# Kernel tuning notes

Hardware: AMD Instinct MI355X
Metric: run time of the kernel (lower is better)

Reference implementation:

```python
import jax, jax.numpy as jnp
import numpy as np

DIM = 512

def setup_inputs() -> dict:
    key = jax.random.key(0)
    ks = jax.random.split(key, 7)
    B, Nq, Nkv = 8, 1024, 4096
    prototype = jax.random.normal(ks[0], (B, Nq, DIM), dtype=jnp.float32)
    q_x = jax.random.normal(ks[1], (B, Nkv, DIM), dtype=jnp.float32)
    qry_attn_mask = jax.random.bernoulli(ks[2], 0.5, (B, Nkv))  # True = keep
    # Linear(dim, dim, bias=False) weights, torch convention y = x @ W.T
    s = 1.0 / np.sqrt(DIM)
    Wq = jax.random.uniform(ks[3], (DIM, DIM), jnp.float32, -s, s)
    Wk = jax.random.uniform(ks[4], (DIM, DIM), jnp.float32, -s, s)
    Wv = jax.random.uniform(ks[5], (DIM, DIM), jnp.float32, -s, s)
    Wproj = jax.random.uniform(ks[6], (DIM, DIM), jnp.float32, -s, s)
    return {"prototype": prototype, "q_x": q_x, "qry_attn_mask": qry_attn_mask,
            "Wq": Wq, "Wk": Wk, "Wv": Wv, "Wproj": Wproj}

def reference(prototype, q_x, qry_attn_mask, Wq, Wk, Wv, Wproj):
    scale = DIM ** (-0.5)
    q = jnp.einsum('bnd,ed->bne', prototype, Wq)          # [B,Nq,D]
    k = jnp.einsum('bmd,ed->bme', q_x, Wk)                # [B,Nkv,D]
    v = jnp.einsum('bmd,ed->bme', q_x, Wv)                # [B,Nkv,D]
    attn = jnp.einsum('bnd,bmd->bnm', q, k) * scale       # [B,Nq,Nkv]
    bias = (~qry_attn_mask).astype(attn.dtype)[:, None, :] * -10000.0
    attn = jax.nn.softmax(attn + bias, axis=-1)
    x = jnp.einsum('bnm,bmd->bnd', attn, v)
    x = jnp.einsum('bnd,ed->bne', x, Wproj)
    return x
```

## Files before the change

### kernel.cpp

```cpp
#include <hip/hip_runtime.h>
#include <hip/hip_bf16.h>
#include <stdint.h>


typedef __bf16 bf16;
typedef bf16 bf16x8 __attribute__((ext_vector_type(8)));
typedef bf16 bf16x4 __attribute__((ext_vector_type(4)));
typedef float f32x4 __attribute__((ext_vector_type(4)));

#define NB 8
#define NQ 1024
#define NKV 4096
#define DD 512
#define RT_LD 136

__device__ __forceinline__ void direct16(const void* g, void* s) {
  __builtin_amdgcn_global_load_lds(
      (const __attribute__((address_space(1))) void*)g,
      (__attribute__((address_space(3))) void*)s, 16, 0, 0);
}

__global__ void cvt_kernel(const float* __restrict__ src, bf16* __restrict__ dst, int n4) {
  int i = blockIdx.x * blockDim.x + threadIdx.x;
  if (i < n4) {
    float4 v = ((const float4*)src)[i];
    bf16x4 o;
    o.x = (bf16)v.x; o.y = (bf16)v.y; o.z = (bf16)v.z; o.w = (bf16)v.w;
    ((bf16x4*)dst)[i] = o;
  }
}

__global__ void cvt_weights(const float* __restrict__ Wq, const float* __restrict__ Wk,
                            const float* __restrict__ Wv, const float* __restrict__ Wp,
                            bf16* __restrict__ Wq_b, bf16* __restrict__ Wkv_b,
                            bf16* __restrict__ Wp_b) {
  int i = blockIdx.x * blockDim.x + threadIdx.x;
  int w = i >> 16, r = i & 65535;
  const float* src = (w == 0) ? Wq : (w == 1) ? Wk : (w == 2) ? Wv : Wp;
  bf16x4* dst = (w == 0) ? (bf16x4*)Wq_b
              : (w == 3) ? (bf16x4*)Wp_b
                         : (bf16x4*)Wkv_b + (w == 2 ? 65536 : 0);
  float4 v = ((const float4*)src)[r];
  bf16x4 o;
  o.x = (bf16)v.x; o.y = (bf16)v.y; o.z = (bf16)v.z; o.w = (bf16)v.w;
  dst[r] = o;
}

__global__ void sniff_zero(const unsigned* __restrict__ mask, int* __restrict__ flag,
                           float* __restrict__ denom) {
  __shared__ int s_bad0, s_bad1;
  if (threadIdx.x == 0) { s_bad0 = 0; s_bad1 = 0; }
  __syncthreads();
  int b0 = 0, b1 = 0;
  for (int i = threadIdx.x; i < 8192; i += 256) {
    unsigned v = mask[i];
    if (v > 1u) b0 = 1;
    if (v != 0u && v != 0x3F800000u) b1 = 1;
  }
  if (b0) atomicOr(&s_bad0, 1);
  if (b1) atomicOr(&s_bad1, 1);
  for (int i = threadIdx.x; i < NB * NQ; i += 256) denom[i] = 0.f;
  __syncthreads();
  if (threadIdx.x == 0) *flag = (s_bad0 == 0) ? 0 : ((s_bad1 == 0) ? 1 : 2);
}

__global__ void scan_mask(const void* __restrict__ mask, const int* __restrict__ flagP,
                          int* __restrict__ idx, int* __restrict__ cnt,
                          int* __restrict__ kpad) {
  const int b = blockIdx.x, tid = threadIdx.x;
  const int mode = *flagP;
  __shared__ int ps[256];
  unsigned bits = 0;
  int c = 0;
  const int base = tid * 16;
  for (int i = 0; i < 16; ++i) {
    const int col = base + i;
    bool k;
    if (mode == 0)      k = ((const int*)mask)[b * NKV + col] != 0;
    else if (mode == 1) k = ((const float*)mask)[b * NKV + col] != 0.f;
    else                k = ((const unsigned char*)mask)[b * NKV + col] != 0;
    bits |= (unsigned)k << i;
    c += k;
  }
  ps[tid] = c;
  __syncthreads();
  for (int s = 1; s < 256; s <<= 1) {
    int v = (tid >= s) ? ps[tid - s] : 0;
    __syncthreads();
    ps[tid] += v;
    __syncthreads();
  }
  int off = ps[tid] - c;
  for (int i = 0; i < 16; ++i)
    if ((bits >> i) & 1) idx[b * NKV + off++] = base + i;
  if (tid == 255) {
    cnt[b] = ps[255];
    kpad[b] = (ps[255] + 127) & ~127;
  }
}

__global__ void gather_qx(const float* __restrict__ qx, const int* __restrict__ idx,
                          const int* __restrict__ cnt, bf16* __restrict__ qc) {
  const int b = blockIdx.y;
  const int wave = threadIdx.x >> 6, lane = threadIdx.x & 63;
  const int r0 = blockIdx.x * 16 + wave * 4;
  const int n = cnt[b];
#pragma unroll
  for (int j = 0; j < 4; ++j) {
    const int row = r0 + j;
    if (row >= n) return;
    const int src = idx[b * NKV + row];
    const float4* s = (const float4*)(qx + ((long)b * NKV + src) * DD) + lane;
    bf16x4* d = (bf16x4*)(qc + ((long)b * NKV + row) * DD) + lane;
    float4 v0 = s[0], v1 = s[64];
    bf16x4 o0, o1;
    o0.x = (bf16)v0.x; o0.y = (bf16)v0.y; o0.z = (bf16)v0.z; o0.w = (bf16)v0.w;
    o1.x = (bf16)v1.x; o1.y = (bf16)v1.y; o1.z = (bf16)v1.z; o1.w = (bf16)v1.w;
    d[0] = o0;
    d[64] = o1;
  }
}

template <int EPI>
__global__ void __launch_bounds__(256, 2)
gemm_bt(const bf16* __restrict__ A, const bf16* __restrict__ Bw,
        void* __restrict__ Cp, void* __restrict__ Cp2,
        int N, int Klen, int Kstride,
        long sA, long sB, long sC,
        const int* __restrict__ cnt, const int* __restrict__ kpad,
        float* __restrict__ denom, float scale, int M) {
  __shared__ alignas(16) bf16 Smem[128 * RT_LD];
  bf16* As = Smem;
  bf16* Bs = Smem + 4096;
  bf16* Rt = Smem;
  const int tid = threadIdx.x;
  const int wave = tid >> 6, lane = tid & 63;
  const int l15 = lane & 15, l4 = lane >> 4;
  const int wm = (wave >> 1) * 64, wn = (wave & 1) * 64;
  const int bx = (EPI == 5) ? blockIdx.y : blockIdx.x;
  const int by = (EPI == 5) ? blockIdx.x : blockIdx.y;
  const int b = blockIdx.z;

  if constexpr (EPI == 2) {
    if (bx * 128 >= kpad[b]) return;
  } else {
    const int bb = by >> 5, loc = (by & 31) * 128;
    if (loc >= kpad[bb]) return;
  }

  const bf16* Ab = A + (long)b * sA + (long)(by * 128) * Kstride;
  const bf16* Bb = Bw + (long)b * sB + (long)(bx * 128) * Kstride;

  const int c0 = wave * 2, c1 = wave * 2 + 1;
  const int srow = lane >> 2;
  const int scol = (lane & 3) * 8;
  const bf16* ag0 = Ab + (long)(c0 * 16 + srow) * Kstride + scol;
  const bf16* ag1 = Ab + (long)(c1 * 16 + srow) * Kstride + scol;
  const bf16* bg0 = Bb + (long)(c0 * 16 + srow) * Kstride + scol;
  const bf16* bg1 = Bb + (long)(c1 * 16 + srow) * Kstride + scol;
  bf16* al0 = As + c0 * 512 + lane * 8;
  bf16* al1 = As + c1 * 512 + lane * 8;
  bf16* bl0 = Bs + c0 * 512 + lane * 8;
  bf16* bl1 = Bs + c1 * 512 + lane * 8;

  f32x4 acc[4][4] = {};

  for (int kt = 0; kt < Klen; kt += 32) {
    __syncthreads();
    direct16(ag0, al0);
    direct16(ag1, al1);
    direct16(bg0, bl0);
    direct16(bg1, bl1);
    ag0 += 32; ag1 += 32; bg0 += 32; bg1 += 32;
    __syncthreads();
    bf16x8 af[4], bfr[4];
#pragma unroll
    for (int t = 0; t < 4; ++t)
      af[t] = *(const bf16x8*)(As + (wm + t * 16 + l15) * 32 + l4 * 8);
#pragma unroll
    for (int t = 0; t < 4; ++t)
      bfr[t] = *(const bf16x8*)(Bs + (wn + t * 16 + l15) * 32 + l4 * 8);
#pragma unroll
    for (int mt = 0; mt < 4; ++mt)
#pragma unroll
      for (int nt = 0; nt < 4; ++nt)
        acc[mt][nt] = __builtin_amdgcn_mfma_f32_16x16x32_bf16(af[mt], bfr[nt],
                                                              acc[mt][nt], 0, 0, 0);
  }

  const int rowBase = by * 128 + wm;
  const int colBase = bx * 128 + wn;
  const int tR = by * 128;
  const int tC = bx * 128;

  if constexpr (EPI == 2) {
    __syncthreads();
    bf16* C = (bf16*)Cp + (long)b * sC;
    const int nkeep = cnt[b];
    float rs[4][4];
#pragma unroll
    for (int mt = 0; mt < 4; ++mt)
#pragma unroll
      for (int r = 0; r < 4; ++r) rs[mt][r] = 0.f;
#pragma unroll
    for (int nt = 0; nt < 4; ++nt) {
      const bool keep = (colBase + nt * 16 + l15) < nkeep;
#pragma unroll
      for (int mt = 0; mt < 4; ++mt)
#pragma unroll
        for (int r = 0; r < 4; ++r) {
          float p = keep ? __expf(acc[mt][nt][r] * scale) : 0.f;
          rs[mt][r] += p;
          Rt[(wm + mt * 16 + l4 * 4 + r) * RT_LD + wn + nt * 16 + l15] = (bf16)p;
        }
    }
#pragma unroll
    for (int mt = 0; mt < 4; ++mt)
#pragma unroll
      for (int r = 0; r < 4; ++r) {
        float v = rs[mt][r];
        v += __shfl_xor(v, 1, 64);
        v += __shfl_xor(v, 2, 64);
        v += __shfl_xor(v, 4, 64);
        v += __shfl_xor(v, 8, 64);
        if (l15 == 0)
          atomicAdd(&denom[b * M + rowBase + mt * 16 + l4 * 4 + r], v);
      }
    __syncthreads();
    const int r0 = tid >> 2, cq = (tid & 3) * 32;
#pragma unroll
    for (int h = 0; h < 128; h += 64)
#pragma unroll
      for (int j = 0; j < 4; ++j) {
        bf16x8 v = *(const bf16x8*)(Rt + (r0 + h) * RT_LD + cq + j * 8);
        *(bf16x8*)(C + (long)(tR + r0 + h) * N + tC + cq + j * 8) = v;
      }
  } else {
    __syncthreads();
    if (tC < 512) {
      bf16* C = (bf16*)Cp;
#pragma unroll
      for (int mt = 0; mt < 4; ++mt)
#pragma unroll
        for (int nt = 0; nt < 4; ++nt)
#pragma unroll
          for (int r = 0; r < 4; ++r)
            Rt[(wm + mt * 16 + l4 * 4 + r) * RT_LD + wn + nt * 16 + l15] =
                (bf16)acc[mt][nt][r];
      __syncthreads();
      const int r0 = tid >> 2, cq = (tid & 3) * 32;
#pragma unroll
      for (int h = 0; h < 128; h += 64)
#pragma unroll
        for (int j = 0; j < 4; ++j) {
          bf16x8 v = *(const bf16x8*)(Rt + (r0 + h) * RT_LD + cq + j * 8);
          *(bf16x8*)(C + (long)(tR + r0 + h) * 512 + tC + cq + j * 8) = v;
        }
    } else {
      bf16* C = (bf16*)Cp2;
#pragma unroll
      for (int mt = 0; mt < 4; ++mt) {
        const int r0 = wm + mt * 16 + l4 * 4;
#pragma unroll
        for (int nt = 0; nt < 4; ++nt) {
          const int cloc = wn + nt * 16 + l15;
          bf16x4 o;
          o.x = (bf16)acc[mt][nt][0]; o.y = (bf16)acc[mt][nt][1];
          o.z = (bf16)acc[mt][nt][2]; o.w = (bf16)acc[mt][nt][3];
          *(bf16x4*)(Rt + cloc * RT_LD + r0) = o;
        }
      }
      __syncthreads();
      const int bb = tR >> 12, kvloc = tR & 4095;
      const int d0 = tid >> 2, kvq = (tid & 3) * 32;
#pragma unroll
      for (int h = 0; h < 128; h += 64)
#pragma unroll
        for (int j = 0; j < 4; ++j) {
          bf16x8 v = *(const bf16x8*)(Rt + (d0 + h) * RT_LD + kvq + j * 8);
          *(bf16x8*)(C + (long)bb * DD * NKV + (long)(tC - 512 + d0 + h) * NKV +
                     kvloc + kvq + j * 8) = v;
        }
    }
  }
}

template <int EPI>
__global__ void __launch_bounds__(256, 4)
gemm_n64(const bf16* __restrict__ A, const bf16* __restrict__ Bw,
         void* __restrict__ Cp) {
  constexpr int SME = (EPI == 0) ? 128 * 72 : 6144;
  __shared__ alignas(16) bf16 Smem[SME];
  bf16* As = Smem;
  bf16* Bs = Smem + 4096;
  bf16* Rt = Smem;
  const int tid = threadIdx.x;
  const int wave = tid >> 6, lane = tid & 63;
  const int l15 = lane & 15, l4 = lane >> 4;
  const int wm = (wave >> 1) * 64, wn = (wave & 1) * 32;

  const bf16* Ab = A + (long)(blockIdx.y * 128) * DD;
  const bf16* Bb = Bw + (long)(blockIdx.x * 64) * DD;

  const int srow = lane >> 2, scol = (lane & 3) * 8;
  const bf16* ag0 = Ab + (long)(wave * 32 + srow) * DD + scol;
  const bf16* ag1 = ag0 + 16 * DD;
  const bf16* bg0 = Bb + (long)(wave * 16 + srow) * DD + scol;
  bf16* al0 = As + wave * 1024 + lane * 8;
  bf16* al1 = al0 + 512;
  bf16* bl0 = Bs + wave * 512 + lane * 8;

  f32x4 acc[4][2] = {};

  for (int kt = 0; kt < DD; kt += 32) {
    __syncthreads();
    direct16(ag0, al0);
    direct16(ag1, al1);
    direct16(bg0, bl0);
    ag0 += 32; ag1 += 32; bg0 += 32;
    __syncthreads();
    bf16x8 af[4], bfr[2];
#pragma unroll
    for (int t = 0; t < 4; ++t)
      af[t] = *(const bf16x8*)(As + (wm + t * 16 + l15) * 32 + l4 * 8);
#pragma unroll
    for (int t = 0; t < 2; ++t)
      bfr[t] = *(const bf16x8*)(Bs + (wn + t * 16 + l15) * 32 + l4 * 8);
#pragma unroll
    for (int mt = 0; mt < 4; ++mt)
#pragma unroll
      for (int nt = 0; nt < 2; ++nt)
        acc[mt][nt] = __builtin_amdgcn_mfma_f32_16x16x32_bf16(af[mt], bfr[nt],
                                                              acc[mt][nt], 0, 0, 0);
  }

  const int tR = blockIdx.y * 128, tC = blockIdx.x * 64;
  if constexpr (EPI == 0) {
    __syncthreads();
#pragma unroll
    for (int mt = 0; mt < 4; ++mt)
#pragma unroll
      for (int nt = 0; nt < 2; ++nt)
#pragma unroll
        for (int r = 0; r < 4; ++r)
          Rt[(wm + mt * 16 + l4 * 4 + r) * 72 + wn + nt * 16 + l15] =
              (bf16)acc[mt][nt][r];
    __syncthreads();
    bf16* C = (bf16*)Cp;
    const int r0 = tid >> 1, cq = (tid & 1) * 32;
#pragma unroll
    for (int j = 0; j < 4; ++j) {
      bf16x8 v = *(const bf16x8*)(Rt + r0 * 72 + cq + j * 8);
      *(bf16x8*)(C + (long)(tR + r0) * DD + tC + cq + j * 8) = v;
    }
  } else {
    float* C = (float*)Cp;
#pragma unroll
    for (int mt = 0; mt < 4; ++mt)
#pragma unroll
      for (int nt = 0; nt < 2; ++nt)
#pragma unroll
        for (int r = 0; r < 4; ++r)
          C[(long)(tR + wm + mt * 16 + l4 * 4 + r) * DD + tC + wn + nt * 16 + l15] =
              acc[mt][nt][r];
  }
}

__global__ void __launch_bounds__(256, 4)
pv_direct(const bf16* __restrict__ P, const bf16* __restrict__ vT,
          const float* __restrict__ denom, const int* __restrict__ kpad,
          bf16* __restrict__ x) {
  __shared__ alignas(16) bf16 Smem[64 * RT_LD];
  bf16* As = Smem;
  bf16* Bs = Smem + 2048;
  bf16* Rt = Smem;
  const int tid = threadIdx.x;
  const int wave = tid >> 6, lane = tid & 63;
  const int l15 = lane & 15, l4 = lane >> 4;
  const int wm = (wave >> 1) * 32, wn = (wave & 1) * 64;
  const int qB = blockIdx.x * 64;
  const int dB = blockIdx.y * 128;
  const int b = blockIdx.z;
  const int Kb = kpad[b];

  const bf16* Ab = P + (long)b * NQ * NKV + (long)qB * NKV;
  const bf16* Bb = vT + (long)b * DD * NKV + (long)dB * NKV;

  const int srow = lane >> 2, scol = (lane & 3) * 8;
  const bf16* ag = Ab + (long)(wave * 16 + srow) * NKV + scol;
  const bf16* bg0 = Bb + (long)(wave * 32 + srow) * NKV + scol;
  const bf16* bg1 = bg0 + 16 * NKV;
  bf16* al = As + wave * 512 + lane * 8;
  bf16* bl0 = Bs + wave * 1024 + lane * 8;
  bf16* bl1 = bl0 + 512;

  f32x4 acc[2][4] = {};

  for (int kt = 0; kt < Kb; kt += 32) {
    __syncthreads();
    direct16(ag, al);
    direct16(bg0, bl0);
    direct16(bg1, bl1);
    ag += 32; bg0 += 32; bg1 += 32;
    __syncthreads();
    bf16x8 af[2], bfr[4];
#pragma unroll
    for (int t = 0; t < 2; ++t)
      af[t] = *(const bf16x8*)(As + (wm + t * 16 + l15) * 32 + l4 * 8);
#pragma unroll
    for (int t = 0; t < 4; ++t)
      bfr[t] = *(const bf16x8*)(Bs + (wn + t * 16 + l15) * 32 + l4 * 8);
#pragma unroll
    for (int mt = 0; mt < 2; ++mt)
#pragma unroll
      for (int nt = 0; nt < 4; ++nt)
        acc[mt][nt] = __builtin_amdgcn_mfma_f32_16x16x32_bf16(af[mt], bfr[nt],
                                                              acc[mt][nt], 0, 0, 0);
  }

  __syncthreads();
#pragma unroll
  for (int mt = 0; mt < 2; ++mt)
#pragma unroll
    for (int r = 0; r < 4; ++r) {
      const int row = wm + mt * 16 + l4 * 4 + r;
      const float inv = 1.0f / denom[b * NQ + qB + row];
#pragma unroll
      for (int nt = 0; nt < 4; ++nt)
        Rt[row * RT_LD + wn + nt * 16 + l15] = (bf16)(acc[mt][nt][r] * inv);
    }
  __syncthreads();
  const int r0 = tid >> 2, cq = (tid & 3) * 32;
#pragma unroll
  for (int j = 0; j < 4; ++j) {
    bf16x8 v = *(const bf16x8*)(Rt + r0 * RT_LD + cq + j * 8);
    *(bf16x8*)(x + (long)(b * NQ + qB + r0) * DD + dB + cq + j * 8) = v;
  }
}

extern "C" void kernel_launch(void* const* d_in, const int* in_sizes, int n_in,
                              void* d_out, int out_size, void* d_ws, size_t ws_size,
                              hipStream_t stream) {
  const float* proto = (const float*)d_in[0];
  const float* qx    = (const float*)d_in[1];
  const void*  mask  = d_in[2];
  const float* Wq    = (const float*)d_in[3];
  const float* Wk    = (const float*)d_in[4];
  const float* Wv    = (const float*)d_in[5];
  const float* Wproj = (const float*)d_in[6];
  float* out = (float*)d_out;

  char* w = (char*)d_ws;
  int*   flag  = (int*)w;
  int*   cnt   = (int*)(w + 64);
  int*   kpadA = (int*)(w + 128);
  float* denom = (float*)(w + 4096);
  size_t off = 65536;
  bf16* Wq_b  = (bf16*)(w + off); off += (size_t)DD * DD * 2;
  bf16* Wkv_b = (bf16*)(w + off); off += (size_t)DD * DD * 4;
  bf16* Wp_b  = (bf16*)(w + off); off += (size_t)DD * DD * 2;
  int*  idx   = (int*)(w + off);  off += (size_t)NB * NKV * 4;
  bf16* q_b   = (bf16*)(w + off); off += (size_t)NB * NQ * DD * 2;
  bf16* k_b   = (bf16*)(w + off); off += (size_t)NB * NKV * DD * 2;
  bf16* vT_b  = (bf16*)(w + off); off += (size_t)NB * NKV * DD * 2;
  bf16* x_b   = (bf16*)(w + off); off += (size_t)NB * NQ * DD * 2;
  size_t off_pp = off;
  bf16* proto_b = (bf16*)(w + off); off += (size_t)NB * NQ * DD * 2;
  bf16* qc_b    = (bf16*)(w + off);
  bf16* P       = (bf16*)(w + off_pp);

  sniff_zero<<<1, 256, 0, stream>>>((const unsigned*)mask, flag, denom);
  scan_mask<<<8, 256, 0, stream>>>(mask, flag, idx, cnt, kpadA);

  cvt_kernel<<<NB * NQ * DD / 4 / 256, 256, 0, stream>>>(proto, proto_b, NB * NQ * DD / 4);
  gather_qx<<<dim3(NKV / 16, NB), 256, 0, stream>>>(qx, idx, cnt, qc_b);
  cvt_weights<<<4 * 65536 / 256, 256, 0, stream>>>(Wq, Wk, Wv, Wproj, Wq_b, Wkv_b, Wp_b);

  const float scale = 0.04419417382415922f;

  gemm_n64<0><<<dim3(8, 64, 1), 256, 0, stream>>>(proto_b, Wq_b, q_b);
  gemm_bt<5><<<dim3(256, 8, 1), 256, 0, stream>>>(
      qc_b, Wkv_b, k_b, vT_b, 1024, DD, DD, 0L, 0L, 0L,
      cnt, kpadA, nullptr, 0.f, 0);
  gemm_bt<2><<<dim3(NKV / 128, NQ / 128, NB), 256, 0, stream>>>(
      q_b, k_b, P, nullptr, NKV, DD, DD,
      (long)NQ * DD, (long)NKV * DD, (long)NQ * NKV,
      cnt, kpadA, denom, scale, NQ);
  pv_direct<<<dim3(16, 4, 8), 256, 0, stream>>>(P, vT_b, denom, kpadA, x_b);
  gemm_n64<4><<<dim3(8, 64, 1), 256, 0, stream>>>(x_b, Wp_b, out);
}
```

Baseline: 341.6 us.

## Halve gemm_bt epilogue LDS via two-pass staging and shrink PV tile to 32 rows

The gemm_bt epilogue now stages the 128x128 output tile through LDS in two 64-row (or 64-column) halves. This halves the shared-memory footprint and lets launch bounds rise to 4 blocks per CU. The pv_direct kernel drops from 64 to 32 query rows per block, doubling the grid and cutting LDS use to give more parallelism across CUs. The cost is extra barriers in the epilogue, and in PV each V tile load is amortised over fewer rows, which raises global traffic for vT.

```diff
diff --git a/kernel.cpp b/kernel.cpp
--- a/kernel.cpp
+++ b/kernel.cpp
@@ -122,14 +122,14 @@
 }
 
 template <int EPI>
-__global__ void __launch_bounds__(256, 2)
+__global__ void __launch_bounds__(256, 4)
 gemm_bt(const bf16* __restrict__ A, const bf16* __restrict__ Bw,
         void* __restrict__ Cp, void* __restrict__ Cp2,
         int N, int Klen, int Kstride,
         long sA, long sB, long sC,
         const int* __restrict__ cnt, const int* __restrict__ kpad,
         float* __restrict__ denom, float scale, int M) {
-  __shared__ alignas(16) bf16 Smem[128 * RT_LD];
+  __shared__ alignas(16) bf16 Smem[64 * RT_LD];
   bf16* As = Smem;
   bf16* Bs = Smem + 4096;
   bf16* Rt = Smem;
@@ -193,94 +193,106 @@
   const int tR = by * 128;
   const int tC = bx * 128;
 
+  __syncthreads();
+
   if constexpr (EPI == 2) {
-    __syncthreads();
     bf16* C = (bf16*)Cp + (long)b * sC;
     const int nkeep = cnt[b];
-    float rs[4][4];
-#pragma unroll
-    for (int mt = 0; mt < 4; ++mt)
-#pragma unroll
-      for (int r = 0; r < 4; ++r) rs[mt][r] = 0.f;
-#pragma unroll
-    for (int nt = 0; nt < 4; ++nt) {
-      const bool keep = (colBase + nt * 16 + l15) < nkeep;
-#pragma unroll
-      for (int mt = 0; mt < 4; ++mt)
-#pragma unroll
-        for (int r = 0; r < 4; ++r) {
-          float p = keep ? __expf(acc[mt][nt][r] * scale) : 0.f;
-          rs[mt][r] += p;
-          Rt[(wm + mt * 16 + l4 * 4 + r) * RT_LD + wn + nt * 16 + l15] = (bf16)p;
+#pragma unroll
+    for (int h2 = 0; h2 < 2; ++h2) {
+      if (wm == h2 * 64) {
+        float rs[4][4];
+#pragma unroll
+        for (int mt = 0; mt < 4; ++mt)
+#pragma unroll
+          for (int r = 0; r < 4; ++r) rs[mt][r] = 0.f;
+#pragma unroll
+        for (int nt = 0; nt < 4; ++nt) {
+          const bool keep = (colBase + nt * 16 + l15) < nkeep;
+#pragma unroll
+          for (int mt = 0; mt < 4; ++mt)
+#pragma unroll
+            for (int r = 0; r < 4; ++r) {
+              float p = keep ? __expf(acc[mt][nt][r] * scale) : 0.f;
+              rs[mt][r] += p;
+              Rt[(mt * 16 + l4 * 4 + r) * RT_LD + wn + nt * 16 + l15] = (bf16)p;
+            }
         }
+#pragma unroll
+        for (int mt = 0; mt < 4; ++mt)
+#pragma unroll
+          for (int r = 0; r < 4; ++r) {
+            float v = rs[mt][r];
+            v += __shfl_xor(v, 1, 64);
+            v += __shfl_xor(v, 2, 64);
+            v += __shfl_xor(v, 4, 64);
+            v += __shfl_xor(v, 8, 64);
+            if (l15 == 0)
+              atomicAdd(&denom[b * M + rowBase + mt * 16 + l4 * 4 + r], v);
+          }
+      }
+      __syncthreads();
+      const int r0 = tid >> 2, cq = (tid & 3) * 32;
+#pragma unroll
+      for (int j = 0; j < 4; ++j) {
+        bf16x8 v = *(const bf16x8*)(Rt + r0 * RT_LD + cq + j * 8);
+        *(bf16x8*)(C + (long)(tR + h2 * 64 + r0) * N + tC + cq + j * 8) = v;
+      }
+      __syncthreads();
     }
-#pragma unroll
-    for (int mt = 0; mt < 4; ++mt)
-#pragma unroll
-      for (int r = 0; r < 4; ++r) {
-        float v = rs[mt][r];
-        v += __shfl_xor(v, 1, 64);
-        v += __shfl_xor(v, 2, 64);
-        v += __shfl_xor(v, 4, 64);
-        v += __shfl_xor(v, 8, 64);
-        if (l15 == 0)
-          atomicAdd(&denom[b * M + rowBase + mt * 16 + l4 * 4 + r], v);
-      }
-    __syncthreads();
-    const int r0 = tid >> 2, cq = (tid & 3) * 32;
-#pragma unroll
-    for (int h = 0; h < 128; h += 64)
-#pragma unroll
-      for (int j = 0; j < 4; ++j) {
-        bf16x8 v = *(const bf16x8*)(Rt + (r0 + h) * RT_LD + cq + j * 8);
-        *(bf16x8*)(C + (long)(tR + r0 + h) * N + tC + cq + j * 8) = v;
-      }
   } else {
-    __syncthreads();
     if (tC < 512) {
       bf16* C = (bf16*)Cp;
 #pragma unroll
-      for (int mt = 0; mt < 4; ++mt)
-#pragma unroll
-        for (int nt = 0; nt < 4; ++nt)
-#pragma unroll
-          for (int r = 0; r < 4; ++r)
-            Rt[(wm + mt * 16 + l4 * 4 + r) * RT_LD + wn + nt * 16 + l15] =
-                (bf16)acc[mt][nt][r];
-      __syncthreads();
-      const int r0 = tid >> 2, cq = (tid & 3) * 32;
-#pragma unroll
-      for (int h = 0; h < 128; h += 64)
+      for (int h2 = 0; h2 < 2; ++h2) {
+        if (wm == h2 * 64) {
+#pragma unroll
+          for (int mt = 0; mt < 4; ++mt)
+#pragma unroll
+            for (int nt = 0; nt < 4; ++nt)
+#pragma unroll
+              for (int r = 0; r < 4; ++r)
+                Rt[(mt * 16 + l4 * 4 + r) * RT_LD + wn + nt * 16 + l15] =
+                    (bf16)acc[mt][nt][r];
+        }
+        __syncthreads();
+        const int r0 = tid >> 2, cq = (tid & 3) * 32;
 #pragma unroll
         for (int j = 0; j < 4; ++j) {
-          bf16x8 v = *(const bf16x8*)(Rt + (r0 + h) * RT_LD + cq + j * 8);
-          *(bf16x8*)(C + (long)(tR + r0 + h) * 512 + tC + cq + j * 8) = v;
+          bf16x8 v = *(const bf16x8*)(Rt + r0 * RT_LD + cq + j * 8);
+          *(bf16x8*)(C + (long)(tR + h2 * 64 + r0) * 512 + tC + cq + j * 8) = v;
         }
+        __syncthreads();
+      }
     } else {
       bf16* C = (bf16*)Cp2;
-#pragma unroll
-      for (int mt = 0; mt < 4; ++mt) {
-        const int r0 = wm + mt * 16 + l4 * 4;
-#pragma unroll
-        for (int nt = 0; nt < 4; ++nt) {
-          const int cloc = wn + nt * 16 + l15;
-          bf16x4 o;
-          o.x = (bf16)acc[mt][nt][0]; o.y = (bf16)acc[mt][nt][1];
-          o.z = (bf16)acc[mt][nt][2]; o.w = (bf16)acc[mt][nt][3];
-          *(bf16x4*)(Rt + cloc * RT_LD + r0) = o;
+      const int bb = tR >> 12, kvloc = tR & 4095;
+#pragma unroll
+      for (int h2 = 0; h2 < 2; ++h2) {
+        if (wn == h2 * 64) {
+#pragma unroll
+          for (int mt = 0; mt < 4; ++mt) {
+            const int r0k = wm + mt * 16 + l4 * 4;
+#pragma unroll
+            for (int nt = 0; nt < 4; ++nt) {
+              const int dl = nt * 16 + l15;
+              bf16x4 o;
+              o.x = (bf16)acc[mt][nt][0]; o.y = (bf16)acc[mt][nt][1];
+              o.z = (bf16)acc[mt][nt][2]; o.w = (bf16)acc[mt][nt][3];
+              *(bf16x4*)(Rt + dl * RT_LD + r0k) = o;
+            }
+          }
         }
+        __syncthreads();
+        const int d0 = tid >> 2, kvq = (tid & 3) * 32;
+#pragma unroll
+        for (int j = 0; j < 4; ++j) {
+          bf16x8 v = *(const bf16x8*)(Rt + d0 * RT_LD + kvq + j * 8);
+          *(bf16x8*)(C + (long)bb * DD * NKV +
+                     (long)(tC - 512 + h2 * 64 + d0) * NKV + kvloc + kvq + j * 8) = v;
+        }
+        __syncthreads();
       }
-      __syncthreads();
-      const int bb = tR >> 12, kvloc = tR & 4095;
-      const int d0 = tid >> 2, kvq = (tid & 3) * 32;
-#pragma unroll
-      for (int h = 0; h < 128; h += 64)
-#pragma unroll
-        for (int j = 0; j < 4; ++j) {
-          bf16x8 v = *(const bf16x8*)(Rt + (d0 + h) * RT_LD + kvq + j * 8);
-          *(bf16x8*)(C + (long)bb * DD * NKV + (long)(tC - 512 + d0 + h) * NKV +
-                     kvloc + kvq + j * 8) = v;
-        }
     }
   }
 }
@@ -370,15 +382,15 @@
 pv_direct(const bf16* __restrict__ P, const bf16* __restrict__ vT,
           const float* __restrict__ denom, const int* __restrict__ kpad,
           bf16* __restrict__ x) {
-  __shared__ alignas(16) bf16 Smem[64 * RT_LD];
+  __shared__ alignas(16) bf16 Smem[5120];
   bf16* As = Smem;
-  bf16* Bs = Smem + 2048;
+  bf16* Bs = Smem + 1024;
   bf16* Rt = Smem;
   const int tid = threadIdx.x;
   const int wave = tid >> 6, lane = tid & 63;
   const int l15 = lane & 15, l4 = lane >> 4;
-  const int wm = (wave >> 1) * 32, wn = (wave & 1) * 64;
-  const int qB = blockIdx.x * 64;
+  const int wm = (wave >> 1) * 16, wn = (wave & 1) * 64;
+  const int qB = blockIdx.x * 32;
   const int dB = blockIdx.y * 128;
   const int b = blockIdx.z;
   const int Kb = kpad[b];
@@ -388,51 +400,44 @@
 
   const int srow = lane >> 2, scol = (lane & 3) * 8;
   const bf16* ag = Ab + (long)(wave * 16 + srow) * NKV + scol;
+  bf16* al = As + wave * 512 + lane * 8;
   const bf16* bg0 = Bb + (long)(wave * 32 + srow) * NKV + scol;
   const bf16* bg1 = bg0 + 16 * NKV;
-  bf16* al = As + wave * 512 + lane * 8;
   bf16* bl0 = Bs + wave * 1024 + lane * 8;
   bf16* bl1 = bl0 + 512;
 
-  f32x4 acc[2][4] = {};
+  f32x4 acc[4] = {};
 
   for (int kt = 0; kt < Kb; kt += 32) {
     __syncthreads();
-    direct16(ag, al);
+    if (wave < 2) direct16(ag, al);
     direct16(bg0, bl0);
     direct16(bg1, bl1);
     ag += 32; bg0 += 32; bg1 += 32;
     __syncthreads();
-    bf16x8 af[2], bfr[4];
-#pragma unroll
-    for (int t = 0; t < 2; ++t)
-      af[t] = *(const bf16x8*)(As + (wm + t * 16 + l15) * 32 + l4 * 8);
+    bf16x8 af, bfr[4];
+    af = *(const bf16x8*)(As + (wm + l15) * 32 + l4 * 8);
 #pragma unroll
     for (int t = 0; t < 4; ++t)
       bfr[t] = *(const bf16x8*)(Bs + (wn + t * 16 + l15) * 32 + l4 * 8);
 #pragma unroll
-    for (int mt = 0; mt < 2; ++mt)
-#pragma unroll
-      for (int nt = 0; nt < 4; ++nt)
-        acc[mt][nt] = __builtin_amdgcn_mfma_f32_16x16x32_bf16(af[mt], bfr[nt],
-                                                              acc[mt][nt], 0, 0, 0);
-  }
-
-  __syncthreads();
-#pragma unroll
-  for (int mt = 0; mt < 2; ++mt)
-#pragma unroll
-    for (int r = 0; r < 4; ++r) {
-      const int row = wm + mt * 16 + l4 * 4 + r;
-      const float inv = 1.0f / denom[b * NQ + qB + row];
-#pragma unroll
-      for (int nt = 0; nt < 4; ++nt)
-        Rt[row * RT_LD + wn + nt * 16 + l15] = (bf16)(acc[mt][nt][r] * inv);
-    }
-  __syncthreads();
-  const int r0 = tid >> 2, cq = (tid & 3) * 32;
-#pragma unroll
-  for (int j = 0; j < 4; ++j) {
+    for (int nt = 0; nt < 4; ++nt)
+      acc[nt] = __builtin_amdgcn_mfma_f32_16x16x32_bf16(af, bfr[nt], acc[nt], 0, 0, 0);
+  }
+
+  __syncthreads();
+#pragma unroll
+  for (int r = 0; r < 4; ++r) {
+    const int row = wm + l4 * 4 + r;
+    const float inv = 1.0f / denom[b * NQ + qB + row];
+#pragma unroll
+    for (int nt = 0; nt < 4; ++nt)
+      Rt[row * RT_LD + wn + nt * 16 + l15] = (bf16)(acc[nt][r] * inv);
+  }
+  __syncthreads();
+  const int r0 = tid >> 3, cq = (tid & 7) * 16;
+#pragma unroll
+  for (int j = 0; j < 2; ++j) {
     bf16x8 v = *(const bf16x8*)(Rt + r0 * RT_LD + cq + j * 8);
     *(bf16x8*)(x + (long)(b * NQ + qB + r0) * DD + dB + cq + j * 8) = v;
   }
@@ -486,6 +491,6 @@
       q_b, k_b, P, nullptr, NKV, DD, DD,
       (long)NQ * DD, (long)NKV * DD, (long)NQ * NKV,
       cnt, kpadA, denom, scale, NQ);
-  pv_direct<<<dim3(16, 4, 8), 256, 0, stream>>>(P, vT_b, denom, kpadA, x_b);
+  pv_direct<<<dim3(32, 4, 8), 256, 0, stream>>>(P, vT_b, denom, kpadA, x_b);
   gemm_n64<4><<<dim3(8, 64, 1), 256, 0, stream>>>(x_b, Wp_b, out);
 }
```

Result: slower. 353.8 us (+3.6%).

## Replace direct global-to-LDS loads with register-prefetched software pipeline in GEMMs

Applied to the files above, without the earlier changes.

All three GEMM kernels drop the global_load_lds direct copies. Each thread now loads the next K-slice into registers while the current slice is consumed from LDS, then writes those registers to LDS at the start of the next iteration. The aim is to overlap global memory latency with MFMA work, since the old loop stalled on each load before computing. The cost is extra VGPRs and an explicit LDS write per tile, still with a single LDS buffer and two barriers per iteration. The epilogue barrier is hoisted to cover both branches.

```diff
diff --git a/kernel.cpp b/kernel.cpp
--- a/kernel.cpp
+++ b/kernel.cpp
@@ -7,18 +7,13 @@
 typedef bf16 bf16x8 __attribute__((ext_vector_type(8)));
 typedef bf16 bf16x4 __attribute__((ext_vector_type(4)));
 typedef float f32x4 __attribute__((ext_vector_type(4)));
+typedef int4 i4;
 
 #define NB 8
 #define NQ 1024
 #define NKV 4096
 #define DD 512
 #define RT_LD 136
-
-__device__ __forceinline__ void direct16(const void* g, void* s) {
-  __builtin_amdgcn_global_load_lds(
-      (const __attribute__((address_space(1))) void*)g,
-      (__attribute__((address_space(3))) void*)s, 16, 0, 0);
-}
 
 __global__ void cvt_kernel(const float* __restrict__ src, bf16* __restrict__ dst, int n4) {
   int i = blockIdx.x * blockDim.x + threadIdx.x;
@@ -165,13 +160,20 @@
 
   f32x4 acc[4][4] = {};
 
+  i4 ra0 = *(const i4*)ag0, ra1 = *(const i4*)ag1;
+  i4 rb0 = *(const i4*)bg0, rb1 = *(const i4*)bg1;
+
   for (int kt = 0; kt < Klen; kt += 32) {
     __syncthreads();
-    direct16(ag0, al0);
-    direct16(ag1, al1);
-    direct16(bg0, bl0);
-    direct16(bg1, bl1);
-    ag0 += 32; ag1 += 32; bg0 += 32; bg1 += 32;
+    *(i4*)al0 = ra0;
+    *(i4*)al1 = ra1;
+    *(i4*)bl0 = rb0;
+    *(i4*)bl1 = rb1;
+    if (kt + 32 < Klen) {
+      ag0 += 32; ag1 += 32; bg0 += 32; bg1 += 32;
+      ra0 = *(const i4*)ag0; ra1 = *(const i4*)ag1;
+      rb0 = *(const i4*)bg0; rb1 = *(const i4*)bg1;
+    }
     __syncthreads();
     bf16x8 af[4], bfr[4];
 #pragma unroll
@@ -193,8 +195,9 @@
   const int tR = by * 128;
   const int tC = bx * 128;
 
+  __syncthreads();
+
   if constexpr (EPI == 2) {
-    __syncthreads();
     bf16* C = (bf16*)Cp + (long)b * sC;
     const int nkeep = cnt[b];
     float rs[4][4];
@@ -236,7 +239,6 @@
         *(bf16x8*)(C + (long)(tR + r0 + h) * N + tC + cq + j * 8) = v;
       }
   } else {
-    __syncthreads();
     if (tC < 512) {
       bf16* C = (bf16*)Cp;
 #pragma unroll
@@ -312,12 +314,17 @@
 
   f32x4 acc[4][2] = {};
 
+  i4 ra0 = *(const i4*)ag0, ra1 = *(const i4*)ag1, rb0 = *(const i4*)bg0;
+
   for (int kt = 0; kt < DD; kt += 32) {
     __syncthreads();
-    direct16(ag0, al0);
-    direct16(ag1, al1);
-    direct16(bg0, bl0);
-    ag0 += 32; ag1 += 32; bg0 += 32;
+    *(i4*)al0 = ra0;
+    *(i4*)al1 = ra1;
+    *(i4*)bl0 = rb0;
+    if (kt + 32 < DD) {
+      ag0 += 32; ag1 += 32; bg0 += 32;
+      ra0 = *(const i4*)ag0; ra1 = *(const i4*)ag1; rb0 = *(const i4*)bg0;
+    }
     __syncthreads();
     bf16x8 af[4], bfr[2];
 #pragma unroll
@@ -396,12 +403,17 @@
 
   f32x4 acc[2][4] = {};
 
+  i4 ra = *(const i4*)ag, rb0 = *(const i4*)bg0, rb1 = *(const i4*)bg1;
+
   for (int kt = 0; kt < Kb; kt += 32) {
     __syncthreads();
-    direct16(ag, al);
-    direct16(bg0, bl0);
-    direct16(bg1, bl1);
-    ag += 32; bg0 += 32; bg1 += 32;
+    *(i4*)al = ra;
+    *(i4*)bl0 = rb0;
+    *(i4*)bl1 = rb1;
+    if (kt + 32 < Kb) {
+      ag += 32; bg0 += 32; bg1 += 32;
+      ra = *(const i4*)ag; rb0 = *(const i4*)bg0; rb1 = *(const i4*)bg1;
+    }
     __syncthreads();
     bf16x8 af[2], bfr[4];
 #pragma unroll
```

New measurement: 324.7 us. 1.05x faster.
